# Kernel tuning notes

Measured on AMD Instinct MI355X. Metric: run time of the kernel, lower is better.

The kernel has to match this reference:

```python
import math
import jax, jax.numpy as jnp
import numpy as np

B, L, H, E = 8, 256, 128, 32


def setup_inputs() -> dict:
    key = jax.random.key(0)
    ks = jax.random.split(key, 24)

    def w(k, shape, fan_in):
        return jax.random.normal(k, shape, jnp.float32) / np.float32(np.sqrt(fan_in))

    inp = {
        "h": jax.random.normal(ks[0], (B, L, H), jnp.float32),
        "edge_feat": jax.random.normal(ks[1], (B, L, L, E), jnp.float32),
        "valid_mask": jax.random.randint(ks[2], (B, L), 0, 2) > 0,
        # edge_proj: Linear(E,H) -> ReLU -> Linear(H,H)
        "We1": w(ks[3], (E, H), E), "be1": jnp.zeros((H,), jnp.float32),
        "We2": w(ks[4], (H, H), H), "be2": jnp.zeros((H,), jnp.float32),
        # att_proj: Linear(3H,H) -> Tanh -> Linear(H,1)
        "Wa1": w(ks[5], (3 * H, H), 3 * H), "ba1": jnp.zeros((H,), jnp.float32),
        "Wa2": w(ks[6], (H, 1), H), "ba2": jnp.zeros((1,), jnp.float32),
        # msg_proj: Linear(2H,H) -> ReLU -> Linear(H,H)
        "Wm1": w(ks[7], (2 * H, H), 2 * H), "bm1": jnp.zeros((H,), jnp.float32),
        "Wm2": w(ks[8], (H, H), H), "bm2": jnp.zeros((H,), jnp.float32),
        # out_proj: Linear(2H,H) -> ReLU -> Linear(H,H)
        "Wo1": w(ks[9], (2 * H, H), 2 * H), "bo1": jnp.zeros((H,), jnp.float32),
        "Wo2": w(ks[10], (H, H), H), "bo2": jnp.zeros((H,), jnp.float32),
        # LayerNorm(H)
        "gamma": jnp.ones((H,), jnp.float32),
        "beta": jnp.zeros((H,), jnp.float32),
    }
    return inp


def _forward(h, edge_feat, valid_mask, We1, be1, We2, be2, Wa1, ba1, Wa2, ba2,
             Wm1, bm1, Wm2, bm2, Wo1, bo1, Wo2, bo2, gamma, beta):
    hd = h.shape[-1]
    # edge MLP: [B,L,L,E] -> [B,L,L,H]
    edge_h = jax.nn.relu(edge_feat @ We1 + be1) @ We2 + be2

    # att_proj on cat([src, dst, edge_h]) == split-weight form (exact same math,
    # avoids materializing the [B,L,L,3H] concat):
    Wa_src, Wa_dst, Wa_edge = Wa1[:hd], Wa1[hd:2 * hd], Wa1[2 * hd:]
    a_src = h @ Wa_src            # [B,L,H], varies over query i
    a_dst = h @ Wa_dst            # [B,L,H], varies over key j
    att_hidden = jnp.tanh(a_src[:, :, None, :] + a_dst[:, None, :, :]
                          + edge_h @ Wa_edge + ba1)      # [B,L,L,H]
    att = (jnp.einsum('bijh,h->bij', att_hidden, Wa2[:, 0]) + ba2[0])
    att = att / np.float32(math.sqrt(hd))

    # masked_fill on invalid keys (dim -1) and invalid queries (dim 1)
    pair_valid = valid_mask[:, :, None] & valid_mask[:, None, :]  # [B,L,L]
    att = jnp.where(pair_valid, att, jnp.float32(-1e9))
    weights = jax.nn.softmax(att, axis=-1)                        # [B,L,L]

    # msg_proj on cat([src, edge_h]); note src[b,i,j] = h[b,i] (query-side)
    Wm_src, Wm_edge = Wm1[:hd], Wm1[hd:]
    msg = jax.nn.relu((h @ Wm_src)[:, :, None, :] + edge_h @ Wm_edge + bm1) @ Wm2 + bm2

    agg = jnp.einsum('bij,bijh->bih', weights, msg)               # [B,L,H]

    # out_proj on cat([h, agg])
    out = jax.nn.relu(h @ Wo1[:hd] + agg @ Wo1[hd:] + bo1) @ Wo2 + bo2

    # residual + LayerNorm (dropout=0 / eval)
    res = h + out
    mu = jnp.mean(res, axis=-1, keepdims=True)
    var = jnp.var(res, axis=-1, keepdims=True)
    normed = (res - mu) * jax.lax.rsqrt(var + jnp.float32(1e-5)) * gamma + beta
    return normed * valid_mask[..., None].astype(normed.dtype)


def reference(h, edge_feat, valid_mask, We1, be1, We2, be2, Wa1, ba1, Wa2, ba2,
              Wm1, bm1, Wm2, bm2, Wo1, bo1, Wo2, bo2, gamma, beta):
    return _forward(h, edge_feat, valid_mask, We1, be1, We2, be2, Wa1, ba1, Wa2,
                    ba2, Wm1, bm1, Wm2, bm2, Wo1, bo1, Wo2, bo2, gamma, beta)
```

## Files before the change

kernel.cpp:

```cpp
#include <hip/hip_runtime.h>


typedef __attribute__((ext_vector_type(8))) short bhalf8;
typedef __attribute__((ext_vector_type(4))) float f32x4;

__device__ __forceinline__ short f2bf(float f) {
  union { float f; unsigned u; } v; v.f = f;
  unsigned r = (v.u + 0x7FFFu + ((v.u >> 16) & 1u)) >> 16;
  return (short)r;
}
__device__ __forceinline__ unsigned cvt_pk(float lo, float hi) {
  unsigned r;
  asm("v_cvt_pk_bf16_f32 %0, %1, %2" : "=v"(r) : "v"(lo), "v"(hi));
  return r;
}
__device__ __forceinline__ float rawexp2(float x) {
  float r;
  asm("v_exp_f32 %0, %1" : "=v"(r) : "v"(x));
  return r;
}
__device__ __forceinline__ float rawrcp(float x) {
  float r;
  asm("v_rcp_f32 %0, %1" : "=v"(r) : "v"(x));
  return r;
}
__device__ __forceinline__ float bf2f(unsigned short x) {
  union { unsigned u; float f; } t; t.u = ((unsigned)x) << 16; return t.f;
}
__device__ __forceinline__ f32x4 mfma16(bhalf8 a, bhalf8 b, f32x4 c) {
  return __builtin_amdgcn_mfma_f32_16x16x32_bf16(a, b, c, 0, 0, 0);
}

__global__ __launch_bounds__(256) void fusedPre(
    const float* __restrict__ hsrc, const int* __restrict__ vmask,
    const float* __restrict__ We1, const float* __restrict__ We2,
    const float* __restrict__ be2, const float* __restrict__ Wa1,
    const float* __restrict__ ba1, const float* __restrict__ Wm1,
    const float* __restrict__ bm1,
    short* __restrict__ we1p, short* __restrict__ weap, short* __restrict__ wemp,
    float* __restrict__ bea, float* __restrict__ bem,
    int* __restrict__ compact, int* __restrict__ bstart, int* __restrict__ cnt,
    float* __restrict__ asrcb, unsigned short* __restrict__ adst_bf,
    float* __restrict__ hmb) {
  __shared__ float shf[8][128];
  __shared__ int wsum[4];
  const int blk = blockIdx.x;
  const int tid = threadIdx.x;

  if (blk < 145) {
    int u = blk * 256 + tid;
    if (u < 4096) {
      int e = u & 7, lane = (u >> 3) & 63, nt = u >> 9;
      int k = 8 * (lane >> 4) + e;
      int n = 64 * (nt >> 2) + 4 * (lane & 15) + (nt & 3);
      we1p[u] = f2bf(We1[k * 128 + n]);
    } else if (u < 20480) {
      int v = u - 4096;
      int e = v & 7, lane = (v >> 3) & 63, nt = (v >> 9) & 7, ks = v >> 12;
      int k = 32 * ks + 8 * (lane >> 4) + e;
      int co = 64 * (nt >> 2) + 4 * (lane & 15) + (nt & 3);
      float a0 = 0.f, a1 = 0.f, a2 = 0.f, a3 = 0.f;
      for (int c = 0; c < 128; c += 4) {
        const float4 w4 = *(const float4*)&We2[k * 128 + c];
        a0 = fmaf(w4.x, Wa1[(256 + c + 0) * 128 + co], a0);
        a1 = fmaf(w4.y, Wa1[(256 + c + 1) * 128 + co], a1);
        a2 = fmaf(w4.z, Wa1[(256 + c + 2) * 128 + co], a2);
        a3 = fmaf(w4.w, Wa1[(256 + c + 3) * 128 + co], a3);
      }
      weap[v] = f2bf((a0 + a1) + (a2 + a3));
    } else if (u < 36864) {
      int v = u - 20480;
      int e = v & 7, lane = (v >> 3) & 63, nt = (v >> 9) & 7, ks = v >> 12;
      int k = 32 * ks + 8 * (lane >> 4) + e;
      int co = 64 * (nt >> 2) + 4 * (lane & 15) + (nt & 3);
      float a0 = 0.f, a1 = 0.f, a2 = 0.f, a3 = 0.f;
      for (int c = 0; c < 128; c += 4) {
        const float4 w4 = *(const float4*)&We2[k * 128 + c];
        a0 = fmaf(w4.x, Wm1[(128 + c + 0) * 128 + co], a0);
        a1 = fmaf(w4.y, Wm1[(128 + c + 1) * 128 + co], a1);
        a2 = fmaf(w4.z, Wm1[(128 + c + 2) * 128 + co], a2);
        a3 = fmaf(w4.w, Wm1[(128 + c + 3) * 128 + co], a3);
      }
      wemp[v] = f2bf((a0 + a1) + (a2 + a3));
    } else if (u < 36992) {
      int hc = u - 36864;
      float acc = ba1[hc];
      for (int c = 0; c < 128; ++c)
        acc = fmaf(be2[c], Wa1[(256 + c) * 128 + hc], acc);
      bea[hc] = acc;
    } else if (u < 37120) {
      int hc = u - 36992;
      float acc = bm1[hc];
      for (int c = 0; c < 128; ++c)
        acc = fmaf(be2[c], Wm1[(128 + c) * 128 + hc], acc);
      bem[hc] = acc;
    }
  } else if (blk == 145) {
    int loc[8], c = 0;
#pragma unroll
    for (int q = 0; q < 8; ++q) {
      int v = vmask[tid * 8 + q] != 0;
      loc[q] = v;
      c += v;
    }
    const int l = tid & 63, w = tid >> 6;
    int pre = c;
#pragma unroll
    for (int o = 1; o < 64; o <<= 1) {
      int t = __shfl_up(pre, o);
      if (l >= o) pre += t;
    }
    if (l == 63) wsum[w] = pre;
    __syncthreads();
    int base = 0;
    for (int q = 0; q < w; ++q) base += wsum[q];
    int off = base + pre - c;
    if ((tid & 31) == 0) bstart[tid >> 5] = off;
#pragma unroll
    for (int q = 0; q < 8; ++q)
      if (loc[q]) compact[off++] = tid * 8 + q;
    if (tid == 255) { cnt[0] = off; bstart[8] = off; }
  } else {
    const int base = (blk - 146) * 8;
    const int col = tid & 127, half = tid >> 7;
#pragma unroll
    for (int g = 0; g < 4; ++g)
      shf[half * 4 + g][col] = hsrc[(size_t)(base + half * 4 + g) * 128 + col];
    __syncthreads();
    float aS[4], aD[4], aM[4];
#pragma unroll
    for (int g = 0; g < 4; ++g) { aS[g] = 0.f; aD[g] = 0.f; aM[g] = 0.f; }
    for (int k = 0; k < 128; k += 4) {
      float s0 = Wa1[(k + 0) * 128 + col], s1 = Wa1[(k + 1) * 128 + col];
      float s2 = Wa1[(k + 2) * 128 + col], s3 = Wa1[(k + 3) * 128 + col];
      float d0 = Wa1[(128 + k + 0) * 128 + col], d1 = Wa1[(128 + k + 1) * 128 + col];
      float d2 = Wa1[(128 + k + 2) * 128 + col], d3 = Wa1[(128 + k + 3) * 128 + col];
      float m0 = Wm1[(k + 0) * 128 + col], m1 = Wm1[(k + 1) * 128 + col];
      float m2 = Wm1[(k + 2) * 128 + col], m3 = Wm1[(k + 3) * 128 + col];
#pragma unroll
      for (int g = 0; g < 4; ++g) {
        const float4 hv = *(const float4*)&shf[half * 4 + g][k];
        aS[g] = fmaf(hv.x, s0, fmaf(hv.y, s1, fmaf(hv.z, s2, fmaf(hv.w, s3, aS[g]))));
        aD[g] = fmaf(hv.x, d0, fmaf(hv.y, d1, fmaf(hv.z, d2, fmaf(hv.w, d3, aD[g]))));
        aM[g] = fmaf(hv.x, m0, fmaf(hv.y, m1, fmaf(hv.z, m2, fmaf(hv.w, m3, aM[g]))));
      }
    }
#pragma unroll
    for (int g = 0; g < 4; ++g) {
      size_t o = (size_t)(base + half * 4 + g) * 128 + col;
      asrcb[o] = aS[g];
      adst_bf[o] = (unsigned short)f2bf(aD[g]);
      hmb[o] = aM[g];
    }
  }
}

__global__ __launch_bounds__(256) void kernC(
    const float* __restrict__ ef, const int* __restrict__ compact,
    const int* __restrict__ bstart, const int* __restrict__ cnt,
    const short* __restrict__ we1p, const short* __restrict__ weap,
    const short* __restrict__ wemp, const float* __restrict__ asrcb,
    const unsigned short* __restrict__ adst_bf, const float* __restrict__ hmb,
    const float* __restrict__ wa2, const float* __restrict__ be1,
    const float* __restrict__ ba2, const float* __restrict__ bea,
    const float* __restrict__ bem, float* __restrict__ aggp,
    float2* __restrict__ msbuf) {
  const int nv = cnt[0];
  const int v = blockIdx.x >> 2;
  if (v >= nv) return;
  const int q = blockIdx.x & 3;
  const int blk = compact[v];
  const int b = blk >> 8;
  const int jb0 = bstart[b];
  const int nb = bstart[b + 1] - jb0;
  if (q * 64 >= nb) return;
  const int tid = threadIdx.x;

  __shared__ short Tl[64 * 128];
  __shared__ float att2[2][64];
  __shared__ float wtil[64];
  __shared__ __align__(16) float asr_s[128], hm_s[128], wa2_s[128];
  __shared__ __align__(16) float be1_s[128];
  __shared__ __align__(16) float agg2[2][128];

  const int w = tid >> 6, l = tid & 63;
  const int l15 = l & 15, l4 = l >> 4;
  const int jh = w >> 1, hh = w & 1;

  float4 f0[2], f1[2];
#pragma unroll
  for (int m = 0; m < 2; ++m) {
    int idx = q * 64 + 32 * jh + 16 * m + l15;
    int jr = compact[jb0 + (idx < nb ? idx : nb - 1)] & 255;
    const float* p = ef + (((size_t)blk * 256 + jr) * 32 + 8 * l4);
    f0[m] = *(const float4*)p;
    f1[m] = *(const float4*)(p + 4);
  }

  if (tid < 128) {
    asr_s[tid] = asrcb[(size_t)blk * 128 + tid] + bea[tid];
    hm_s[tid] = hmb[(size_t)blk * 128 + tid] + bem[tid];
    wa2_s[tid] = wa2[tid];
    be1_s[tid] = be1[tid];
  }
  __syncthreads();

  const float ba2v = ba2[0];
  const float RS = 0.08838834764831845f;
  const f32x4 vz = {0.f, 0.f, 0.f, 0.f};
  const f32x4 asv = *(const f32x4*)&asr_s[hh * 64 + 4 * l15];
  const f32x4 wav = *(const f32x4*)&wa2_s[hh * 64 + 4 * l15];
  const f32x4 b4 = *(const f32x4*)&be1_s[hh * 64 + 4 * l15];
  float whalf = wav[0] + wav[1] + wav[2] + wav[3];
  whalf += __shfl_xor(whalf, 1);
  whalf += __shfl_xor(whalf, 2);
  whalf += __shfl_xor(whalf, 4);
  whalf += __shfl_xor(whalf, 8);

  {
    f32x4 acc[2][4];
#pragma unroll
    for (int m = 0; m < 2; ++m)
#pragma unroll
      for (int n = 0; n < 4; ++n) acc[m][n] = vz;
#pragma unroll
    for (int m = 0; m < 2; ++m) {
      union { bhalf8 v8; unsigned u[4]; } a;
      a.u[0] = cvt_pk(f0[m].x, f0[m].y);
      a.u[1] = cvt_pk(f0[m].z, f0[m].w);
      a.u[2] = cvt_pk(f1[m].x, f1[m].y);
      a.u[3] = cvt_pk(f1[m].z, f1[m].w);
#pragma unroll
      for (int n = 0; n < 4; ++n) {
        bhalf8 bfr = *(const bhalf8*)(we1p + (size_t)((hh * 4 + n) * 64 + l) * 8);
        acc[m][n] = mfma16(a.v8, bfr, acc[m][n]);
      }
    }
#pragma unroll
    for (int m = 0; m < 2; ++m)
#pragma unroll
      for (int r = 0; r < 4; ++r) {
        int jl = 32 * jh + 16 * m + 4 * l4 + r;
        float v0 = fmaxf(acc[m][0][r] + b4[0], 0.f);
        float v1 = fmaxf(acc[m][1][r] + b4[1], 0.f);
        float v2 = fmaxf(acc[m][2][r] + b4[2], 0.f);
        float v3 = fmaxf(acc[m][3][r] + b4[3], 0.f);
        uint2 pk;
        pk.x = cvt_pk(v0, v1);
        pk.y = cvt_pk(v2, v3);
        int byte = (jl * 256 + 128 * hh + 8 * l15) ^ ((jl & 7) << 4);
        *(uint2*)((char*)Tl + byte) = pk;
      }
  }
  __syncthreads();

  {
    ushort4 adp[2][4];
#pragma unroll
    for (int m = 0; m < 2; ++m)
#pragma unroll
      for (int r = 0; r < 4; ++r) {
        int idx = q * 64 + 32 * jh + 16 * m + 4 * l4 + r;
        int jg = compact[jb0 + (idx < nb ? idx : nb - 1)] & 255;
        adp[m][r] = *(const ushort4*)(adst_bf + (size_t)(b * 256 + jg) * 128 +
                                      hh * 64 + 4 * l15);
      }
    f32x4 acc[2][4];
#pragma unroll
    for (int m = 0; m < 2; ++m)
#pragma unroll
      for (int n = 0; n < 4; ++n) acc[m][n] = vz;
#pragma unroll
    for (int ks = 0; ks < 4; ++ks) {
      bhalf8 af[2];
#pragma unroll
      for (int m = 0; m < 2; ++m) {
        int jl = 32 * jh + 16 * m + l15;
        int byte = (jl * 256 + ks * 64 + 16 * l4) ^ ((jl & 7) << 4);
        af[m] = *(const bhalf8*)((const char*)Tl + byte);
      }
#pragma unroll
      for (int n = 0; n < 4; ++n) {
        bhalf8 bf2 = *(const bhalf8*)(weap + (size_t)((ks * 8 + hh * 4 + n) * 64 + l) * 8);
#pragma unroll
        for (int m = 0; m < 2; ++m) acc[m][n] = mfma16(af[m], bf2, acc[m][n]);
      }
    }
#pragma unroll
    for (int m = 0; m < 2; ++m)
#pragma unroll
      for (int r = 0; r < 4; ++r) {
        float racc = 0.f;
        float adv[4] = {bf2f(adp[m][r].x), bf2f(adp[m][r].y),
                        bf2f(adp[m][r].z), bf2f(adp[m][r].w)};
#pragma unroll
        for (int n = 0; n < 4; ++n) {
          float x = acc[m][n][r] + asv[n] + adv[n];
          float e = rawexp2(x * 2.885390082f);
          racc = fmaf(wav[n], rawrcp(e + 1.f), racc);
        }
        racc += __shfl_xor(racc, 1);
        racc += __shfl_xor(racc, 2);
        racc += __shfl_xor(racc, 4);
        racc += __shfl_xor(racc, 8);
        if (l15 == 0)
          att2[hh][32 * jh + 16 * m + 4 * l4 + r] = whalf - 2.f * racc;
      }
  }
  __syncthreads();

  if (w == 0) {
    int idx = q * 64 + l;
    float s = (idx < nb) ? (att2[0][l] + att2[1][l] + ba2v) * RS : -1e30f;
    float mx = s;
#pragma unroll
    for (int o = 1; o < 64; o <<= 1) mx = fmaxf(mx, __shfl_xor(mx, o));
    float e = __expf(s - mx);
    wtil[l] = e;
    float sm = e;
#pragma unroll
    for (int o = 1; o < 64; o <<= 1) sm += __shfl_xor(sm, o);
    if (l == 0) msbuf[blk * 4 + q] = make_float2(mx, sm);
  }
  __syncthreads();

  {
    const f32x4 hv = *(const f32x4*)&hm_s[hh * 64 + 4 * l15];
    f32x4 acc[2][4];
#pragma unroll
    for (int m = 0; m < 2; ++m)
#pragma unroll
      for (int n = 0; n < 4; ++n) acc[m][n] = vz;
#pragma unroll
    for (int ks = 0; ks < 4; ++ks) {
      bhalf8 af[2];
#pragma unroll
      for (int m = 0; m < 2; ++m) {
        int jl = 32 * jh + 16 * m + l15;
        int byte = (jl * 256 + ks * 64 + 16 * l4) ^ ((jl & 7) << 4);
        af[m] = *(const bhalf8*)((const char*)Tl + byte);
      }
#pragma unroll
      for (int n = 0; n < 4; ++n) {
        bhalf8 bf2 = *(const bhalf8*)(wemp + (size_t)((ks * 8 + hh * 4 + n) * 64 + l) * 8);
#pragma unroll
        for (int m = 0; m < 2; ++m) acc[m][n] = mfma16(af[m], bf2, acc[m][n]);
      }
    }
    float part[4] = {0.f, 0.f, 0.f, 0.f};
#pragma unroll
    for (int m = 0; m < 2; ++m)
#pragma unroll
      for (int r = 0; r < 4; ++r) {
        int jl = 32 * jh + 16 * m + 4 * l4 + r;
        float wj = wtil[jl];
#pragma unroll
        for (int n = 0; n < 4; ++n) {
          float vv = fmaxf(acc[m][n][r] + hv[n], 0.f);
          part[n] = fmaf(wj, vv, part[n]);
        }
      }
#pragma unroll
    for (int n = 0; n < 4; ++n) {
      part[n] += __shfl_xor(part[n], 16);
      part[n] += __shfl_xor(part[n], 32);
    }
    if (l4 == 0) {
      f32x4 pv = {part[0], part[1], part[2], part[3]};
      *(f32x4*)&agg2[jh][hh * 64 + 4 * l15] = pv;
    }
  }
  __syncthreads();
  if (tid < 128)
    aggp[((size_t)blk * 4 + q) * 128 + tid] = agg2[0][tid] + agg2[1][tid];
}

__global__ __launch_bounds__(1024) void kernD(
    const float* __restrict__ hsrc, const int* __restrict__ vmask,
    const int* __restrict__ bstart, const float* __restrict__ aggp,
    const float2* __restrict__ msbuf, const float* __restrict__ Wm2,
    const float* __restrict__ bm2, const float* __restrict__ Wo1,
    const float* __restrict__ bo1, const float* __restrict__ Wo2,
    const float* __restrict__ bo2, const float* __restrict__ gma,
    const float* __restrict__ bta, float* __restrict__ outp) {
  __shared__ float hL[8][128], xL[8][128], uL[8][128], rL[8][128];
  __shared__ float2 lnr[8][2];
  const int tid = threadIdx.x;
  const int col = tid & 127, g = tid >> 7;
  const int base = blockIdx.x * 8;
  const int node = base + g;

  hL[g][col] = hsrc[(size_t)node * 128 + col];
  float xv = 0.f;
  if (vmask[node]) {
    const int bb = node >> 8;
    const int nb = bstart[bb + 1] - bstart[bb];
    const int nq = (nb + 63) >> 6;
    float2 ms0 = msbuf[node * 4 + 0];
    float2 ms1 = nq > 1 ? msbuf[node * 4 + 1] : make_float2(-1e30f, 0.f);
    float2 ms2 = nq > 2 ? msbuf[node * 4 + 2] : make_float2(-1e30f, 0.f);
    float2 ms3 = nq > 3 ? msbuf[node * 4 + 3] : make_float2(-1e30f, 0.f);
    float m = fmaxf(fmaxf(ms0.x, ms1.x), fmaxf(ms2.x, ms3.x));
    float w0 = __expf(ms0.x - m), w1 = __expf(ms1.x - m);
    float w2 = __expf(ms2.x - m), w3 = __expf(ms3.x - m);
    float den = w0 * ms0.y + w1 * ms1.y + w2 * ms2.y + w3 * ms3.y;
    size_t ab = (size_t)node * 512 + col;
    float num = w0 * aggp[ab];
    if (nq > 1) num += w1 * aggp[ab + 128];
    if (nq > 2) num += w2 * aggp[ab + 256];
    if (nq > 3) num += w3 * aggp[ab + 384];
    xv = num / den;
  }
  xL[g][col] = xv;
  __syncthreads();

  float a = 0.f;
#pragma unroll 8
  for (int k = 0; k < 128; k += 4) {
    const float4 x4 = *(const float4*)&xL[g][k];
    a = fmaf(x4.x, Wm2[(k + 0) * 128 + col], a);
    a = fmaf(x4.y, Wm2[(k + 1) * 128 + col], a);
    a = fmaf(x4.z, Wm2[(k + 2) * 128 + col], a);
    a = fmaf(x4.w, Wm2[(k + 3) * 128 + col], a);
  }
  uL[g][col] = a + bm2[col];
  __syncthreads();

  a = 0.f;
#pragma unroll 8
  for (int k = 0; k < 128; k += 4) {
    const float4 h4 = *(const float4*)&hL[g][k];
    a = fmaf(h4.x, Wo1[(k + 0) * 128 + col], a);
    a = fmaf(h4.y, Wo1[(k + 1) * 128 + col], a);
    a = fmaf(h4.z, Wo1[(k + 2) * 128 + col], a);
    a = fmaf(h4.w, Wo1[(k + 3) * 128 + col], a);
  }
#pragma unroll 8
  for (int k = 0; k < 128; k += 4) {
    const float4 u4 = *(const float4*)&uL[g][k];
    a = fmaf(u4.x, Wo1[(128 + k + 0) * 128 + col], a);
    a = fmaf(u4.y, Wo1[(128 + k + 1) * 128 + col], a);
    a = fmaf(u4.z, Wo1[(128 + k + 2) * 128 + col], a);
    a = fmaf(u4.w, Wo1[(128 + k + 3) * 128 + col], a);
  }
  rL[g][col] = fmaxf(a + bo1[col], 0.f);
  __syncthreads();

  a = 0.f;
#pragma unroll 8
  for (int k = 0; k < 128; k += 4) {
    const float4 r4 = *(const float4*)&rL[g][k];
    a = fmaf(r4.x, Wo2[(k + 0) * 128 + col], a);
    a = fmaf(r4.y, Wo2[(k + 1) * 128 + col], a);
    a = fmaf(r4.z, Wo2[(k + 2) * 128 + col], a);
    a = fmaf(r4.w, Wo2[(k + 3) * 128 + col], a);
  }
  xL[g][col] = hL[g][col] + a + bo2[col];
  __syncthreads();

  const int w = tid >> 6, l = tid & 63;
  const int gg = w >> 1, hf = w & 1, cc = 64 * hf + l;
  float x = xL[gg][cc];
  float s = x, ss = x * x;
#pragma unroll
  for (int o = 1; o < 64; o <<= 1) {
    s += __shfl_xor(s, o);
    ss += __shfl_xor(ss, o);
  }
  if (l == 0) lnr[gg][hf] = make_float2(s, ss);
  __syncthreads();
  const float2 A = lnr[gg][0], Bv = lnr[gg][1];
  const float S = A.x + Bv.x, SS = A.y + Bv.y;
  const float mu = S * (1.f / 128.f);
  const float var = SS * (1.f / 128.f) - mu * mu;
  const float inv = rsqrtf(var + 1e-5f);
  const int nd = base + gg;
  const int valid = vmask[nd];
  float o0 = valid ? (x - mu) * inv * gma[cc] + bta[cc] : 0.f;
  outp[(size_t)nd * 128 + cc] = o0;
}

extern "C" void kernel_launch(void* const* d_in, const int* in_sizes, int n_in,
                              void* d_out, int out_size, void* d_ws, size_t ws_size,
                              hipStream_t stream) {
  const float* h_in = (const float*)d_in[0];
  const float* ef = (const float*)d_in[1];
  const int* vmask = (const int*)d_in[2];
  const float* We1 = (const float*)d_in[3];
  const float* be1 = (const float*)d_in[4];
  const float* We2 = (const float*)d_in[5];
  const float* be2 = (const float*)d_in[6];
  const float* Wa1 = (const float*)d_in[7];
  const float* ba1 = (const float*)d_in[8];
  const float* Wa2 = (const float*)d_in[9];
  const float* ba2 = (const float*)d_in[10];
  const float* Wm1 = (const float*)d_in[11];
  const float* bm1 = (const float*)d_in[12];
  const float* Wm2 = (const float*)d_in[13];
  const float* bm2 = (const float*)d_in[14];
  const float* Wo1 = (const float*)d_in[15];
  const float* bo1 = (const float*)d_in[16];
  const float* Wo2 = (const float*)d_in[17];
  const float* bo2 = (const float*)d_in[18];
  const float* gma = (const float*)d_in[19];
  const float* bta = (const float*)d_in[20];

  char* ws = (char*)d_ws;
  short* we1p = (short*)(ws + 0);
  short* weap = (short*)(ws + 8192);
  short* wemp = (short*)(ws + 40960);
  float* bea = (float*)(ws + 73728);
  float* bem = (float*)(ws + 74240);
  int* compact = (int*)(ws + 74752);
  int* bstart = (int*)(ws + 82944);
  int* cnt = (int*)(ws + 83072);
  float* asrcb = (float*)(ws + 83136);
  float* hmb = (float*)(ws + 83136 + 1048576);
  unsigned short* adst_bf = (unsigned short*)(ws + 83136 + 2097152);
  float* aggp = (float*)(ws + 83136 + 2621440);
  float2* msbuf = (float2*)(ws + 83136 + 2621440 + 4194304);

  fusedPre<<<dim3(402), dim3(256), 0, stream>>>(
      h_in, vmask, We1, We2, be2, Wa1, ba1, Wm1, bm1, we1p, weap, wemp, bea,
      bem, compact, bstart, cnt, asrcb, adst_bf, hmb);
  kernC<<<dim3(8192), dim3(256), 0, stream>>>(ef, compact, bstart, cnt, we1p,
                                              weap, wemp, asrcb, adst_bf, hmb,
                                              Wa2, be1, ba2, bea, bem, aggp,
                                              msbuf);
  kernD<<<dim3(256), dim3(1024), 0, stream>>>(h_in, vmask, bstart, aggp, msbuf,
                                              Wm2, bm2, Wo1, bo1, Wo2, bo2,
                                              gma, bta, (float*)d_out);
}
```

Measured before the change: 82.71 us.

## Give each wave its own 16-row tile to drop block-wide syncs

Restructures the edge-attention kernel so each of the four waves owns 16 key rows across all 128 hidden columns, where before waves split rows and columns. Each wave builds its own private LDS tile, computes logits, and runs a local online softmax with its own max and sum. The four waves' partial sums are merged once at the end with exp rescaling. This removes three of the four block barriers and the shared staging of bias vectors, at the cost of more accumulator registers per wave (8 fragments) and a few extra exps in the final merge.

```diff
diff --git a/kernel.cpp b/kernel.cpp
--- a/kernel.cpp
+++ b/kernel.cpp
@@ -175,204 +175,202 @@
   const int nb = bstart[b + 1] - jb0;
   if (q * 64 >= nb) return;
   const int tid = threadIdx.x;
-
-  __shared__ short Tl[64 * 128];
-  __shared__ float att2[2][64];
-  __shared__ float wtil[64];
-  __shared__ __align__(16) float asr_s[128], hm_s[128], wa2_s[128];
-  __shared__ __align__(16) float be1_s[128];
-  __shared__ __align__(16) float agg2[2][128];
-
   const int w = tid >> 6, l = tid & 63;
   const int l15 = l & 15, l4 = l >> 4;
-  const int jh = w >> 1, hh = w & 1;
-
-  float4 f0[2], f1[2];
-#pragma unroll
-  for (int m = 0; m < 2; ++m) {
-    int idx = q * 64 + 32 * jh + 16 * m + l15;
-    int jr = compact[jb0 + (idx < nb ? idx : nb - 1)] & 255;
-    const float* p = ef + (((size_t)blk * 256 + jr) * 32 + 8 * l4);
-    f0[m] = *(const float4*)p;
-    f1[m] = *(const float4*)(p + 4);
-  }
-
-  if (tid < 128) {
-    asr_s[tid] = asrcb[(size_t)blk * 128 + tid] + bea[tid];
-    hm_s[tid] = hmb[(size_t)blk * 128 + tid] + bem[tid];
-    wa2_s[tid] = wa2[tid];
-    be1_s[tid] = be1[tid];
-  }
-  __syncthreads();
+
+  __shared__ short Tl[4][16 * 128];
+  __shared__ __align__(16) float aggL[4][128];
+  __shared__ float2 msL[4];
+
+  {
+    int idxT = q * 64 + 16 * w + l15;
+    int jrT = compact[jb0 + (idxT < nb ? idxT : nb - 1)] & 255;
+    const float* p = ef + (((size_t)blk * 256 + jrT) * 32 + 8 * l4);
+    float4 f0 = *(const float4*)p;
+    float4 f1 = *(const float4*)(p + 4);
+
+    const f32x4 b40 = *(const f32x4*)&be1[4 * l15];
+    const f32x4 b41 = *(const f32x4*)&be1[64 + 4 * l15];
+
+    f32x4 acc[8];
+#pragma unroll
+    for (int n = 0; n < 8; ++n) acc[n] = {0.f, 0.f, 0.f, 0.f};
+    union { bhalf8 v8; unsigned u[4]; } a;
+    a.u[0] = cvt_pk(f0.x, f0.y);
+    a.u[1] = cvt_pk(f0.z, f0.w);
+    a.u[2] = cvt_pk(f1.x, f1.y);
+    a.u[3] = cvt_pk(f1.z, f1.w);
+#pragma unroll
+    for (int n = 0; n < 8; ++n) {
+      bhalf8 bfr = *(const bhalf8*)(we1p + (size_t)(n * 64 + l) * 8);
+      acc[n] = mfma16(a.v8, bfr, acc[n]);
+    }
+    char* Tb = (char*)Tl[w];
+#pragma unroll
+    for (int r = 0; r < 4; ++r) {
+      int rr = 4 * l4 + r;
+      float v0 = fmaxf(acc[0][r] + b40[0], 0.f);
+      float v1 = fmaxf(acc[1][r] + b40[1], 0.f);
+      float v2 = fmaxf(acc[2][r] + b40[2], 0.f);
+      float v3 = fmaxf(acc[3][r] + b40[3], 0.f);
+      float v4 = fmaxf(acc[4][r] + b41[0], 0.f);
+      float v5 = fmaxf(acc[5][r] + b41[1], 0.f);
+      float v6 = fmaxf(acc[6][r] + b41[2], 0.f);
+      float v7 = fmaxf(acc[7][r] + b41[3], 0.f);
+      uint2 p0, p1;
+      p0.x = cvt_pk(v0, v1); p0.y = cvt_pk(v2, v3);
+      p1.x = cvt_pk(v4, v5); p1.y = cvt_pk(v6, v7);
+      int swz = (rr & 7) << 4;
+      *(uint2*)(Tb + ((rr * 256 + 8 * l15) ^ swz)) = p0;
+      *(uint2*)(Tb + ((rr * 256 + 128 + 8 * l15) ^ swz)) = p1;
+    }
+  }
 
   const float ba2v = ba2[0];
   const float RS = 0.08838834764831845f;
-  const f32x4 vz = {0.f, 0.f, 0.f, 0.f};
-  const f32x4 asv = *(const f32x4*)&asr_s[hh * 64 + 4 * l15];
-  const f32x4 wav = *(const f32x4*)&wa2_s[hh * 64 + 4 * l15];
-  const f32x4 b4 = *(const f32x4*)&be1_s[hh * 64 + 4 * l15];
-  float whalf = wav[0] + wav[1] + wav[2] + wav[3];
-  whalf += __shfl_xor(whalf, 1);
-  whalf += __shfl_xor(whalf, 2);
-  whalf += __shfl_xor(whalf, 4);
-  whalf += __shfl_xor(whalf, 8);
-
+  const char* Tb = (const char*)Tl[w];
+  const int swzR = (l15 & 7) << 4;
+
+  const f32x4 asv0 = *(const f32x4*)&asrcb[(size_t)blk * 128 + 4 * l15] +
+                     *(const f32x4*)&bea[4 * l15];
+  const f32x4 asv1 = *(const f32x4*)&asrcb[(size_t)blk * 128 + 64 + 4 * l15] +
+                     *(const f32x4*)&bea[64 + 4 * l15];
+  const f32x4 wav0 = *(const f32x4*)&wa2[4 * l15];
+  const f32x4 wav1 = *(const f32x4*)&wa2[64 + 4 * l15];
+  float wtot = (wav0[0] + wav0[1] + wav0[2] + wav0[3]) +
+               (wav1[0] + wav1[1] + wav1[2] + wav1[3]);
+  wtot += __shfl_xor(wtot, 1);
+  wtot += __shfl_xor(wtot, 2);
+  wtot += __shfl_xor(wtot, 4);
+  wtot += __shfl_xor(wtot, 8);
+
+  ushort4 adL[4], adH[4];
+#pragma unroll
+  for (int r = 0; r < 4; ++r) {
+    int idxr = q * 64 + 16 * w + 4 * l4 + r;
+    int jg = compact[jb0 + (idxr < nb ? idxr : nb - 1)] & 255;
+    const unsigned short* ap = adst_bf + (size_t)(b * 256 + jg) * 128;
+    adL[r] = *(const ushort4*)(ap + 4 * l15);
+    adH[r] = *(const ushort4*)(ap + 64 + 4 * l15);
+  }
+
+  float logit[4];
   {
-    f32x4 acc[2][4];
-#pragma unroll
-    for (int m = 0; m < 2; ++m)
-#pragma unroll
-      for (int n = 0; n < 4; ++n) acc[m][n] = vz;
-#pragma unroll
-    for (int m = 0; m < 2; ++m) {
-      union { bhalf8 v8; unsigned u[4]; } a;
-      a.u[0] = cvt_pk(f0[m].x, f0[m].y);
-      a.u[1] = cvt_pk(f0[m].z, f0[m].w);
-      a.u[2] = cvt_pk(f1[m].x, f1[m].y);
-      a.u[3] = cvt_pk(f1[m].z, f1[m].w);
-#pragma unroll
-      for (int n = 0; n < 4; ++n) {
-        bhalf8 bfr = *(const bhalf8*)(we1p + (size_t)((hh * 4 + n) * 64 + l) * 8);
-        acc[m][n] = mfma16(a.v8, bfr, acc[m][n]);
-      }
-    }
-#pragma unroll
-    for (int m = 0; m < 2; ++m)
-#pragma unroll
-      for (int r = 0; r < 4; ++r) {
-        int jl = 32 * jh + 16 * m + 4 * l4 + r;
-        float v0 = fmaxf(acc[m][0][r] + b4[0], 0.f);
-        float v1 = fmaxf(acc[m][1][r] + b4[1], 0.f);
-        float v2 = fmaxf(acc[m][2][r] + b4[2], 0.f);
-        float v3 = fmaxf(acc[m][3][r] + b4[3], 0.f);
-        uint2 pk;
-        pk.x = cvt_pk(v0, v1);
-        pk.y = cvt_pk(v2, v3);
-        int byte = (jl * 256 + 128 * hh + 8 * l15) ^ ((jl & 7) << 4);
-        *(uint2*)((char*)Tl + byte) = pk;
-      }
-  }
+    f32x4 acc[8];
+#pragma unroll
+    for (int n = 0; n < 8; ++n) acc[n] = {0.f, 0.f, 0.f, 0.f};
+#pragma unroll
+    for (int ks = 0; ks < 4; ++ks) {
+      bhalf8 af = *(const bhalf8*)(Tb + ((l15 * 256 + ks * 64 + 16 * l4) ^ swzR));
+#pragma unroll
+      for (int n = 0; n < 8; ++n) {
+        bhalf8 bf2 = *(const bhalf8*)(weap + (size_t)((ks * 8 + n) * 64 + l) * 8);
+        acc[n] = mfma16(af, bf2, acc[n]);
+      }
+    }
+#pragma unroll
+    for (int r = 0; r < 4; ++r) {
+      float racc = 0.f;
+      float ad[8] = {bf2f(adL[r].x), bf2f(adL[r].y), bf2f(adL[r].z),
+                     bf2f(adL[r].w), bf2f(adH[r].x), bf2f(adH[r].y),
+                     bf2f(adH[r].z), bf2f(adH[r].w)};
+      float as[8] = {asv0[0], asv0[1], asv0[2], asv0[3],
+                     asv1[0], asv1[1], asv1[2], asv1[3]};
+      float wv[8] = {wav0[0], wav0[1], wav0[2], wav0[3],
+                     wav1[0], wav1[1], wav1[2], wav1[3]};
+#pragma unroll
+      for (int n = 0; n < 8; ++n) {
+        float x = acc[n][r] + as[n] + ad[n];
+        float e = rawexp2(x * 2.885390082f);
+        racc = fmaf(wv[n], rawrcp(e + 1.f), racc);
+      }
+      racc += __shfl_xor(racc, 1);
+      racc += __shfl_xor(racc, 2);
+      racc += __shfl_xor(racc, 4);
+      racc += __shfl_xor(racc, 8);
+      logit[r] = wtot - 2.f * racc;
+    }
+  }
+
+  float m16, s16, wj[4];
+  {
+    float sc[4];
+#pragma unroll
+    for (int r = 0; r < 4; ++r) {
+      int idxr = q * 64 + 16 * w + 4 * l4 + r;
+      sc[r] = (idxr < nb) ? (logit[r] + ba2v) * RS : -1e30f;
+    }
+    float mx = fmaxf(fmaxf(sc[0], sc[1]), fmaxf(sc[2], sc[3]));
+    mx = fmaxf(mx, __shfl_xor(mx, 16));
+    mx = fmaxf(mx, __shfl_xor(mx, 32));
+    m16 = mx;
+    float sl = 0.f;
+#pragma unroll
+    for (int r = 0; r < 4; ++r) {
+      wj[r] = __expf(sc[r] - m16);
+      sl += wj[r];
+    }
+    sl += __shfl_xor(sl, 16);
+    sl += __shfl_xor(sl, 32);
+    s16 = sl;
+  }
+
+  float part[8] = {0.f, 0.f, 0.f, 0.f, 0.f, 0.f, 0.f, 0.f};
+  {
+    const f32x4 hv0 = *(const f32x4*)&hmb[(size_t)blk * 128 + 4 * l15] +
+                      *(const f32x4*)&bem[4 * l15];
+    const f32x4 hv1 = *(const f32x4*)&hmb[(size_t)blk * 128 + 64 + 4 * l15] +
+                      *(const f32x4*)&bem[64 + 4 * l15];
+    f32x4 acc[8];
+#pragma unroll
+    for (int n = 0; n < 8; ++n) acc[n] = {0.f, 0.f, 0.f, 0.f};
+#pragma unroll
+    for (int ks = 0; ks < 4; ++ks) {
+      bhalf8 af = *(const bhalf8*)(Tb + ((l15 * 256 + ks * 64 + 16 * l4) ^ swzR));
+#pragma unroll
+      for (int n = 0; n < 8; ++n) {
+        bhalf8 bf2 = *(const bhalf8*)(wemp + (size_t)((ks * 8 + n) * 64 + l) * 8);
+        acc[n] = mfma16(af, bf2, acc[n]);
+      }
+    }
+    float hvv[8] = {hv0[0], hv0[1], hv0[2], hv0[3],
+                    hv1[0], hv1[1], hv1[2], hv1[3]};
+#pragma unroll
+    for (int r = 0; r < 4; ++r)
+#pragma unroll
+      for (int n = 0; n < 8; ++n) {
+        float vv = fmaxf(acc[n][r] + hvv[n], 0.f);
+        part[n] = fmaf(wj[r], vv, part[n]);
+      }
+  }
+
+#pragma unroll
+  for (int n = 0; n < 8; ++n) {
+    part[n] += __shfl_xor(part[n], 16);
+    part[n] += __shfl_xor(part[n], 32);
+  }
+  if (l4 == 0) {
+    f32x4 p0 = {part[0], part[1], part[2], part[3]};
+    f32x4 p1 = {part[4], part[5], part[6], part[7]};
+    *(f32x4*)&aggL[w][4 * l15] = p0;
+    *(f32x4*)&aggL[w][64 + 4 * l15] = p1;
+  }
+  if (l == 0) msL[w] = make_float2(m16, s16);
   __syncthreads();
 
-  {
-    ushort4 adp[2][4];
-#pragma unroll
-    for (int m = 0; m < 2; ++m)
-#pragma unroll
-      for (int r = 0; r < 4; ++r) {
-        int idx = q * 64 + 32 * jh + 16 * m + 4 * l4 + r;
-        int jg = compact[jb0 + (idx < nb ? idx : nb - 1)] & 255;
-        adp[m][r] = *(const ushort4*)(adst_bf + (size_t)(b * 256 + jg) * 128 +
-                                      hh * 64 + 4 * l15);
-      }
-    f32x4 acc[2][4];
-#pragma unroll
-    for (int m = 0; m < 2; ++m)
-#pragma unroll
-      for (int n = 0; n < 4; ++n) acc[m][n] = vz;
-#pragma unroll
-    for (int ks = 0; ks < 4; ++ks) {
-      bhalf8 af[2];
-#pragma unroll
-      for (int m = 0; m < 2; ++m) {
-        int jl = 32 * jh + 16 * m + l15;
-        int byte = (jl * 256 + ks * 64 + 16 * l4) ^ ((jl & 7) << 4);
-        af[m] = *(const bhalf8*)((const char*)Tl + byte);
-      }
-#pragma unroll
-      for (int n = 0; n < 4; ++n) {
-        bhalf8 bf2 = *(const bhalf8*)(weap + (size_t)((ks * 8 + hh * 4 + n) * 64 + l) * 8);
-#pragma unroll
-        for (int m = 0; m < 2; ++m) acc[m][n] = mfma16(af[m], bf2, acc[m][n]);
-      }
-    }
-#pragma unroll
-    for (int m = 0; m < 2; ++m)
-#pragma unroll
-      for (int r = 0; r < 4; ++r) {
-        float racc = 0.f;
-        float adv[4] = {bf2f(adp[m][r].x), bf2f(adp[m][r].y),
-                        bf2f(adp[m][r].z), bf2f(adp[m][r].w)};
-#pragma unroll
-        for (int n = 0; n < 4; ++n) {
-          float x = acc[m][n][r] + asv[n] + adv[n];
-          float e = rawexp2(x * 2.885390082f);
-          racc = fmaf(wav[n], rawrcp(e + 1.f), racc);
-        }
-        racc += __shfl_xor(racc, 1);
-        racc += __shfl_xor(racc, 2);
-        racc += __shfl_xor(racc, 4);
-        racc += __shfl_xor(racc, 8);
-        if (l15 == 0)
-          att2[hh][32 * jh + 16 * m + 4 * l4 + r] = whalf - 2.f * racc;
-      }
-  }
-  __syncthreads();
-
-  if (w == 0) {
-    int idx = q * 64 + l;
-    float s = (idx < nb) ? (att2[0][l] + att2[1][l] + ba2v) * RS : -1e30f;
-    float mx = s;
-#pragma unroll
-    for (int o = 1; o < 64; o <<= 1) mx = fmaxf(mx, __shfl_xor(mx, o));
-    float e = __expf(s - mx);
-    wtil[l] = e;
-    float sm = e;
-#pragma unroll
-    for (int o = 1; o < 64; o <<= 1) sm += __shfl_xor(sm, o);
-    if (l == 0) msbuf[blk * 4 + q] = make_float2(mx, sm);
-  }
-  __syncthreads();
-
-  {
-    const f32x4 hv = *(const f32x4*)&hm_s[hh * 64 + 4 * l15];
-    f32x4 acc[2][4];
-#pragma unroll
-    for (int m = 0; m < 2; ++m)
-#pragma unroll
-      for (int n = 0; n < 4; ++n) acc[m][n] = vz;
-#pragma unroll
-    for (int ks = 0; ks < 4; ++ks) {
-      bhalf8 af[2];
-#pragma unroll
-      for (int m = 0; m < 2; ++m) {
-        int jl = 32 * jh + 16 * m + l15;
-        int byte = (jl * 256 + ks * 64 + 16 * l4) ^ ((jl & 7) << 4);
-        af[m] = *(const bhalf8*)((const char*)Tl + byte);
-      }
-#pragma unroll
-      for (int n = 0; n < 4; ++n) {
-        bhalf8 bf2 = *(const bhalf8*)(wemp + (size_t)((ks * 8 + hh * 4 + n) * 64 + l) * 8);
-#pragma unroll
-        for (int m = 0; m < 2; ++m) acc[m][n] = mfma16(af[m], bf2, acc[m][n]);
-      }
-    }
-    float part[4] = {0.f, 0.f, 0.f, 0.f};
-#pragma unroll
-    for (int m = 0; m < 2; ++m)
-#pragma unroll
-      for (int r = 0; r < 4; ++r) {
-        int jl = 32 * jh + 16 * m + 4 * l4 + r;
-        float wj = wtil[jl];
-#pragma unroll
-        for (int n = 0; n < 4; ++n) {
-          float vv = fmaxf(acc[m][n][r] + hv[n], 0.f);
-          part[n] = fmaf(wj, vv, part[n]);
-        }
-      }
-#pragma unroll
-    for (int n = 0; n < 4; ++n) {
-      part[n] += __shfl_xor(part[n], 16);
-      part[n] += __shfl_xor(part[n], 32);
-    }
-    if (l4 == 0) {
-      f32x4 pv = {part[0], part[1], part[2], part[3]};
-      *(f32x4*)&agg2[jh][hh * 64 + 4 * l15] = pv;
-    }
-  }
-  __syncthreads();
-  if (tid < 128)
-    aggp[((size_t)blk * 4 + q) * 128 + tid] = agg2[0][tid] + agg2[1][tid];
+  if (tid < 128) {
+    float2 A0 = msL[0], A1 = msL[1], A2 = msL[2], A3 = msL[3];
+    float m = fmaxf(fmaxf(A0.x, A1.x), fmaxf(A2.x, A3.x));
+    float e0 = __expf(A0.x - m), e1 = __expf(A1.x - m);
+    float e2 = __expf(A2.x - m), e3 = __expf(A3.x - m);
+    float agg = e0 * aggL[0][tid] + e1 * aggL[1][tid] + e2 * aggL[2][tid] +
+                e3 * aggL[3][tid];
+    aggp[((size_t)blk * 4 + q) * 128 + tid] = agg;
+    if (tid == 0) {
+      float s = e0 * A0.y + e1 * A1.y + e2 * A2.y + e3 * A3.y;
+      msbuf[blk * 4 + q] = make_float2(m, s);
+    }
+  }
 }
 
 __global__ __launch_bounds__(1024) void kernD(
```

New measurement: 106.8 us. 1.29x slower.
